# Kernel tuning notes

Measured on AMD Instinct MI355X. Metric: run time of the kernel, lower is better.

Reference implementation:

```python
import jax, jax.numpy as jnp
import numpy as np

N_USER = 50000
N_ITEM = 50000
N_EDGE = 1600000
D_IN = 64
D_OUT = 64


def _mean_agg(msgs, dst, num_dst):
    # copy_u + mean: segment-mean of edge messages onto dst nodes; zero for
    # zero-in-degree nodes (DGL default).
    s = jax.ops.segment_sum(msgs, dst, num_segments=num_dst)          # [Nd, D]
    cnt = jax.ops.segment_sum(jnp.ones((msgs.shape[0],), msgs.dtype), dst,
                              num_segments=num_dst)                    # [Nd]
    return s / jnp.maximum(cnt, 1.0)[:, None]


def setup_inputs() -> dict:
    key = jax.random.key(0)
    ks = jax.random.split(key, 12)
    return {
        'user_feat': jax.random.normal(ks[0], (N_USER, D_IN), jnp.float32),
        'item_feat': jax.random.normal(ks[1], (N_ITEM, D_IN), jnp.float32),
        'rate_src': jax.random.randint(ks[2], (N_EDGE,), 0, N_USER, jnp.int64 if jax.config.jax_enable_x64 else jnp.int32),
        'rate_dst': jax.random.randint(ks[3], (N_EDGE,), 0, N_ITEM, jnp.int64 if jax.config.jax_enable_x64 else jnp.int32),
        'rev_src': jax.random.randint(ks[4], (N_EDGE,), 0, N_ITEM, jnp.int64 if jax.config.jax_enable_x64 else jnp.int32),
        'rev_dst': jax.random.randint(ks[5], (N_EDGE,), 0, N_USER, jnp.int64 if jax.config.jax_enable_x64 else jnp.int32),
        'W_rate': jax.random.normal(ks[6], (D_IN, D_OUT), jnp.float32) * (1.0 / np.sqrt(D_IN)),
        'b_rate': jnp.zeros((D_OUT,), jnp.float32),
        'W_rev': jax.random.normal(ks[7], (D_IN, D_OUT), jnp.float32) * (1.0 / np.sqrt(D_IN)),
        'b_rev': jnp.zeros((D_OUT,), jnp.float32),
        'loop_weight': jax.random.normal(ks[8], (D_IN, D_OUT), jnp.float32) * (1.0 / np.sqrt(D_IN)),
        'h_bias': jnp.zeros((D_OUT,), jnp.float32),
    }


def reference(user_feat, item_feat, rate_src, rate_dst, rev_src, rev_dst,
              W_rate, b_rate, W_rev, b_rev, loop_weight, h_bias):
    # Per-etype Linear on source-node features (applied node-wise, as in torch).
    Wh_rate = user_feat @ W_rate + b_rate      # [Nu, Dout], etype 'rate': user->item
    Wh_rev = item_feat @ W_rev + b_rev         # [Ni, Dout], etype 'rated-by': item->user

    # copy_u + mean per etype, cross-reduce 'sum' (one etype per dst ntype here).
    h_item = _mean_agg(Wh_rate[rate_src], rate_dst, N_ITEM)
    h_user = _mean_agg(Wh_rev[rev_src], rev_dst, N_USER)

    # self-loop + bias (dropout p=0.0 is identity)
    h_user = h_user + user_feat @ loop_weight + h_bias
    h_item = h_item + item_feat @ loop_weight + h_bias
    return (h_user, h_item)
```

## Files before the change

kernel.cpp:

```cpp
#include <hip/hip_runtime.h>

#define N_USER 50000
#define N_ITEM 50000
#define N_NODE 50000
#define N_EDGE 1600000
#define D 64

#define CB_SHIFT 8
#define NBKT 196
#define BCAP 10240
#define CHUNK 8192
#define NCH ((N_EDGE + CHUNK - 1) / CHUNK)
#define NCAST 3125
#define NAGB ((N_NODE + 31) / 32)
#define SA_STR 36

typedef __attribute__((ext_vector_type(8))) short short8;
typedef __attribute__((ext_vector_type(4))) float floatx4;

__device__ __forceinline__ unsigned short f32_to_bf16(float x) {
    unsigned u = __float_as_uint(x);
    unsigned r = (u + 0x7FFFu + ((u >> 16) & 1u)) >> 16;
    return (unsigned short)r;
}
__device__ __forceinline__ unsigned pack2(float lo, float hi) {
    return (unsigned)f32_to_bf16(lo) | ((unsigned)f32_to_bf16(hi) << 16);
}

__device__ __forceinline__ void acc2(float* a, int k, unsigned u) {
    a[k]     += __uint_as_float(u << 16);
    a[k + 1] += __uint_as_float(u & 0xFFFF0000u);
}
__device__ __forceinline__ void acc8(float* a, uint4 w) {
    acc2(a, 0, w.x); acc2(a, 2, w.y); acc2(a, 4, w.z); acc2(a, 6, w.w);
}

__global__ __launch_bounds__(256) void cast_bin(
    const float4* __restrict__ fU, ushort4* __restrict__ bU,
    const float4* __restrict__ fI, ushort4* __restrict__ bI,
    const int* __restrict__ srcA, const int* __restrict__ dstA, unsigned* __restrict__ gbinA,
    const int* __restrict__ srcB, const int* __restrict__ dstB, unsigned* __restrict__ gbinB,
    int* __restrict__ fcur,
    const float* __restrict__ W_rev, const float* __restrict__ W_rate,
    const float* __restrict__ loop_w,
    unsigned short* __restrict__ wtRev, unsigned short* __restrict__ wtRate,
    unsigned short* __restrict__ wtLoop)
{
    __shared__ unsigned lbin[CHUNK];
    __shared__ int hist[NBKT];
    __shared__ int lofs[NBKT];
    __shared__ int lcur[NBKT];
    __shared__ int gbase[NBKT];
    __shared__ int sc[256];

    const int id = blockIdx.x;

    if (id >= 2 * NCH + 2 * NCAST) {
        const int which = id - (2 * NCH + 2 * NCAST);
        const float* __restrict__ Wsrc = which == 0 ? W_rev : (which == 1 ? W_rate : loop_w);
        unsigned short* __restrict__ Wdst = which == 0 ? wtRev : (which == 1 ? wtRate : wtLoop);
        for (int i = threadIdx.x; i < 4096; i += 256)
            Wdst[i] = f32_to_bf16(Wsrc[(i & 63) * 64 + (i >> 6)]);
        return;
    }

    if (id >= 2 * NCH) {
        const int cid = id - 2 * NCH;
        const int et = (cid >= NCAST) ? 1 : 0;
        const float4* __restrict__ in = et ? fI : fU;
        ushort4* __restrict__ out     = et ? bI : bU;
        int i = (cid - et * NCAST) * 256 + threadIdx.x;
        float4 v = in[i];
        ushort4 o;
        o.x = f32_to_bf16(v.x); o.y = f32_to_bf16(v.y);
        o.z = f32_to_bf16(v.z); o.w = f32_to_bf16(v.w);
        out[i] = o;
        return;
    }

    const int et = (id >= NCH) ? 1 : 0;
    const int chunk = id - et * NCH;
    const int* __restrict__ src = et ? srcB : srcA;
    const int* __restrict__ dst = et ? dstB : dstA;
    unsigned* __restrict__ gbin = et ? gbinB : gbinA;
    int* __restrict__ fc = fcur + et * NBKT;

    const int base = chunk * CHUNK;
    const int nE = min(CHUNK, N_EDGE - base);
    const int n4 = nE >> 2;
    const int4* dst4 = (const int4*)(dst + base);
    const int4* src4 = (const int4*)(src + base);
    const int tid = threadIdx.x;

    for (int i = tid; i < NBKT; i += 256) hist[i] = 0;
    __syncthreads();

    for (int i = tid; i < n4; i += 256) {
        int4 d = dst4[i];
        atomicAdd(&hist[d.x >> CB_SHIFT], 1);
        atomicAdd(&hist[d.y >> CB_SHIFT], 1);
        atomicAdd(&hist[d.z >> CB_SHIFT], 1);
        atomicAdd(&hist[d.w >> CB_SHIFT], 1);
    }
    __syncthreads();

    int v = (tid < NBKT) ? hist[tid] : 0;
    sc[tid] = v;
    __syncthreads();
    for (int o = 1; o < 256; o <<= 1) {
        int t = (tid >= o) ? sc[tid - o] : 0;
        __syncthreads();
        sc[tid] += t;
        __syncthreads();
    }
    if (tid < NBKT) {
        int excl = sc[tid] - v;
        lofs[tid] = excl;
        lcur[tid] = excl;
        gbase[tid] = v ? (tid * BCAP + atomicAdd(&fc[tid], v)) : 0;
    }
    __syncthreads();

    for (int i = tid; i < n4; i += 256) {
        int4 d = dst4[i];
        int4 s = src4[i];
        { int p = atomicAdd(&lcur[d.x >> CB_SHIFT], 1); lbin[p] = ((unsigned)d.x << 16) | (unsigned)s.x; }
        { int p = atomicAdd(&lcur[d.y >> CB_SHIFT], 1); lbin[p] = ((unsigned)d.y << 16) | (unsigned)s.y; }
        { int p = atomicAdd(&lcur[d.z >> CB_SHIFT], 1); lbin[p] = ((unsigned)d.z << 16) | (unsigned)s.z; }
        { int p = atomicAdd(&lcur[d.w >> CB_SHIFT], 1); lbin[p] = ((unsigned)d.w << 16) | (unsigned)s.w; }
    }
    __syncthreads();

    const int wv = tid >> 6, ln = tid & 63;
    for (int b = wv; b < NBKT; b += 4) {
        const int s0 = lofs[b], c = hist[b], g = gbase[b];
        for (int t = ln; t < c; t += 64) gbin[g + t] = lbin[s0 + t];
    }
}

__global__ __launch_bounds__(256) void bucket_sort(
    const unsigned* __restrict__ gbinI, unsigned short* __restrict__ srtI,
    int* __restrict__ offI, int* __restrict__ cntI,
    const unsigned* __restrict__ gbinU, unsigned short* __restrict__ srtU,
    int* __restrict__ offU, int* __restrict__ cntU,
    const int* __restrict__ fcur)
{
    const int et = blockIdx.y;
    const unsigned* __restrict__ gbin = et ? gbinU : gbinI;
    unsigned short* __restrict__ srt  = et ? srtU : srtI;
    int* __restrict__ off   = et ? offU : offI;
    int* __restrict__ cntG  = et ? cntU : cntI;
    const int b = blockIdx.x;
    const int startg = b * BCAP;
    const int n = fcur[et * NBKT + b];
    const int nodebase = b << CB_SHIFT;
    const int tid = threadIdx.x;

    __shared__ int cnt[256];
    __shared__ int sc[256];
    __shared__ int pos[256];
    __shared__ unsigned short lsrt[BCAP];

    cnt[tid] = 0;
    __syncthreads();

    for (int i = tid; i < n; i += 256)
        atomicAdd(&cnt[(int)(gbin[startg + i] >> 16) - nodebase], 1);
    __syncthreads();

    int v = cnt[tid];
    sc[tid] = v;
    __syncthreads();
    for (int o = 1; o < 256; o <<= 1) {
        int t = (tid >= o) ? sc[tid - o] : 0;
        __syncthreads();
        sc[tid] += t;
        __syncthreads();
    }
    {
        int excl = sc[tid] - v;
        pos[tid] = excl;
        int node = nodebase + tid;
        if (node < N_NODE) { off[node] = startg + excl; cntG[node] = v; }
    }
    __syncthreads();

    for (int i = tid; i < n; i += 256) {
        unsigned p = gbin[startg + i];
        int q = atomicAdd(&pos[(int)(p >> 16) - nodebase], 1);
        lsrt[q] = (unsigned short)(p & 0xFFFFu);
    }
    __syncthreads();

    for (int i = tid; i < n; i += 256) srt[startg + i] = lsrt[i];
}

__global__ __launch_bounds__(256) void agg_gemm(
    const uint4* __restrict__ userB, const uint4* __restrict__ itemB,
    const int* __restrict__ offU, const int* __restrict__ cntU, const unsigned short* __restrict__ srtU,
    const int* __restrict__ offI, const int* __restrict__ cntI, const unsigned short* __restrict__ srtI,
    const unsigned short* __restrict__ wtRev, const float* __restrict__ b_rev,
    const unsigned short* __restrict__ wtRate, const float* __restrict__ b_rate,
    const unsigned short* __restrict__ wtLoop, const float* __restrict__ h_bias,
    float* __restrict__ out)
{
    const int et = blockIdx.y;
    const uint4* __restrict__ tab = et ? userB : itemB;
    const int* __restrict__ off   = et ? offI : offU;
    const int* __restrict__ cntG  = et ? cntI : cntU;
    const unsigned short* __restrict__ srt = et ? srtI : srtU;
    const unsigned short* __restrict__ Wt  = et ? wtRate : wtRev;
    const float* __restrict__ b_et = et ? b_rate : b_rev;
    const unsigned short* __restrict__ feat =
        (const unsigned short*)(et ? itemB : userB);
    float* __restrict__ outN = out + (et ? (size_t)N_USER * D : 0);

    __shared__ unsigned sA[32][SA_STR];
    __shared__ int sCnt[32];

    const int tid = threadIdx.x;

    const int grp  = tid >> 3;
    const int lane = tid & 7;
    const int node = blockIdx.x * 32 + grp;
    const bool valid = (node < N_NODE);
    const int nd = valid ? node : (N_NODE - 1);
    const int start = off[nd];
    const int c = valid ? cntG[nd] : 0;
    const int end = start + c;

    float aA[8] = {0.f, 0.f, 0.f, 0.f, 0.f, 0.f, 0.f, 0.f};
    float aB[8] = {0.f, 0.f, 0.f, 0.f, 0.f, 0.f, 0.f, 0.f};

    int e = start;
    for (; e + 8 <= end; e += 8) {
        int s0 = (int)srt[e],     s1 = (int)srt[e + 1];
        int s2 = (int)srt[e + 2], s3 = (int)srt[e + 3];
        int s4 = (int)srt[e + 4], s5 = (int)srt[e + 5];
        int s6 = (int)srt[e + 6], s7 = (int)srt[e + 7];
        uint4 w0 = tab[(size_t)s0 * 8 + lane];
        uint4 w1 = tab[(size_t)s1 * 8 + lane];
        uint4 w2 = tab[(size_t)s2 * 8 + lane];
        uint4 w3 = tab[(size_t)s3 * 8 + lane];
        uint4 w4 = tab[(size_t)s4 * 8 + lane];
        uint4 w5 = tab[(size_t)s5 * 8 + lane];
        uint4 w6 = tab[(size_t)s6 * 8 + lane];
        uint4 w7 = tab[(size_t)s7 * 8 + lane];
        acc8(aA, w0); acc8(aB, w1); acc8(aA, w2); acc8(aB, w3);
        acc8(aA, w4); acc8(aB, w5); acc8(aA, w6); acc8(aB, w7);
    }
    for (; e + 4 <= end; e += 4) {
        int s0 = (int)srt[e],     s1 = (int)srt[e + 1];
        int s2 = (int)srt[e + 2], s3 = (int)srt[e + 3];
        uint4 w0 = tab[(size_t)s0 * 8 + lane];
        uint4 w1 = tab[(size_t)s1 * 8 + lane];
        uint4 w2 = tab[(size_t)s2 * 8 + lane];
        uint4 w3 = tab[(size_t)s3 * 8 + lane];
        acc8(aA, w0); acc8(aB, w1); acc8(aA, w2); acc8(aB, w3);
    }
    for (; e < end; ++e) {
        uint4 w = tab[(size_t)(int)srt[e] * 8 + lane];
        acc8(aA, w);
    }
    #pragma unroll
    for (int k = 0; k < 8; ++k) aA[k] += aB[k];

    const float inv = (c > 0) ? 1.0f / (float)c : 0.0f;
    sA[grp][lane * 4 + 0] = pack2(aA[0] * inv, aA[1] * inv);
    sA[grp][lane * 4 + 1] = pack2(aA[2] * inv, aA[3] * inv);
    sA[grp][lane * 4 + 2] = pack2(aA[4] * inv, aA[5] * inv);
    sA[grp][lane * 4 + 3] = pack2(aA[6] * inv, aA[7] * inv);
    if (lane == 0) sCnt[grp] = c;
    __syncthreads();

    const int wave = tid >> 6;
    const int l    = tid & 63;
    const int quad = l >> 4;
    const int l16  = l & 15;
    const int rowbase = (wave & 1) * 16;
    const int colbase = (wave >> 1) * 32;

    const int lrow = rowbase + l16;
    short8 aAgg0 = *(const short8*)&sA[lrow][     quad * 4];
    short8 aAgg1 = *(const short8*)&sA[lrow][16 + quad * 4];
    const int grow = blockIdx.x * 32 + lrow;
    const int gr = (grow < N_NODE) ? grow : (N_NODE - 1);
    short8 aFeat0 = *(const short8*)(feat + (size_t)gr * 64 +      quad * 8);
    short8 aFeat1 = *(const short8*)(feat + (size_t)gr * 64 + 32 + quad * 8);

    #pragma unroll
    for (int t = 0; t < 2; ++t) {
        const int n = colbase + t * 16 + l16;
        short8 bW0 = *(const short8*)(Wt     + n * 64 +      quad * 8);
        short8 bW1 = *(const short8*)(Wt     + n * 64 + 32 + quad * 8);
        short8 bL0 = *(const short8*)(wtLoop + n * 64 +      quad * 8);
        short8 bL1 = *(const short8*)(wtLoop + n * 64 + 32 + quad * 8);
        floatx4 a = {0.f, 0.f, 0.f, 0.f};
        a = __builtin_amdgcn_mfma_f32_16x16x32_bf16(aAgg0,  bW0, a, 0, 0, 0);
        a = __builtin_amdgcn_mfma_f32_16x16x32_bf16(aAgg1,  bW1, a, 0, 0, 0);
        a = __builtin_amdgcn_mfma_f32_16x16x32_bf16(aFeat0, bL0, a, 0, 0, 0);
        a = __builtin_amdgcn_mfma_f32_16x16x32_bf16(aFeat1, bL1, a, 0, 0, 0);
        const float bh = h_bias[n], be = b_et[n];
        #pragma unroll
        for (int i = 0; i < 4; ++i) {
            const int rl = rowbase + quad * 4 + i;
            const int r = blockIdx.x * 32 + rl;
            if (r < N_NODE) {
                outN[(size_t)r * D + n] = a[i] + bh + (sCnt[rl] > 0 ? be : 0.f);
            }
        }
    }
}

extern "C" void kernel_launch(void* const* d_in, const int* in_sizes, int n_in,
                              void* d_out, int out_size, void* d_ws, size_t ws_size,
                              hipStream_t stream)
{
    const float* user_feat = (const float*)d_in[0];
    const float* item_feat = (const float*)d_in[1];
    const int*   rate_src  = (const int*)d_in[2];
    const int*   rate_dst  = (const int*)d_in[3];
    const int*   rev_src   = (const int*)d_in[4];
    const int*   rev_dst   = (const int*)d_in[5];
    const float* W_rate    = (const float*)d_in[6];
    const float* b_rate    = (const float*)d_in[7];
    const float* W_rev     = (const float*)d_in[8];
    const float* b_rev     = (const float*)d_in[9];
    const float* loop_w    = (const float*)d_in[10];
    const float* h_bias    = (const float*)d_in[11];
    float* out = (float*)d_out;

    char* p = (char*)d_ws;
    ushort4* userB = (ushort4*)p; p += (size_t)N_USER * D * 2;
    ushort4* itemB = (ushort4*)p; p += (size_t)N_ITEM * D * 2;
    unsigned* gbinI = (unsigned*)p; p += (size_t)NBKT * BCAP * 4;
    unsigned* gbinU = (unsigned*)p; p += (size_t)NBKT * BCAP * 4;
    unsigned short* srtI = (unsigned short*)p; p += (size_t)NBKT * BCAP * 2;
    unsigned short* srtU = (unsigned short*)p; p += (size_t)NBKT * BCAP * 2;
    int* offI = (int*)p; p += (size_t)N_NODE * 4;
    int* offU = (int*)p; p += (size_t)N_NODE * 4;
    int* cntI = (int*)p; p += (size_t)N_NODE * 4;
    int* cntU = (int*)p; p += (size_t)N_NODE * 4;
    int* fcur = (int*)p; p += (size_t)(2 * NBKT) * 4;
    unsigned short* wtRev  = (unsigned short*)p; p += 4096 * 2;
    unsigned short* wtRate = (unsigned short*)p; p += 4096 * 2;
    unsigned short* wtLoop = (unsigned short*)p; p += 4096 * 2;
    (void)ws_size;

    hipMemsetAsync(fcur, 0, (size_t)(2 * NBKT) * sizeof(int), stream);

    cast_bin<<<dim3(2 * NCH + 2 * NCAST + 3), 256, 0, stream>>>(
        (const float4*)user_feat, userB, (const float4*)item_feat, itemB,
        rate_src, rate_dst, gbinI,
        rev_src,  rev_dst,  gbinU, fcur,
        W_rev, W_rate, loop_w, wtRev, wtRate, wtLoop);

    bucket_sort<<<dim3(NBKT, 2), 256, 0, stream>>>(
        gbinI, srtI, offI, cntI,
        gbinU, srtU, offU, cntU, fcur);

    agg_gemm<<<dim3(NAGB, 2), 256, 0, stream>>>(
        (const uint4*)userB, (const uint4*)itemB,
        offU, cntU, srtU,
        offI, cntI, srtI,
        wtRev, b_rev, wtRate, b_rate,
        wtLoop, h_bias, out);

    (void)in_sizes; (void)n_in; (void)out_size;
}
```

Baseline: 199.9 us.

## Fuse bucket sort into aggregation+GEMM kernel, keeping sorted edges in LDS

Merges the per-bucket counting sort and the gather/mean/MFMA GEMM kernel into one 512-thread kernel. Each bucket is handled by two blocks, each sorting the full bucket into shared memory and then aggregating its half of the nodes from LDS. This removes one kernel launch and the global round trip for the sorted source indices, offsets and counts. The cost is that every bucket is sorted twice, and the larger LDS footprint and fewer blocks lower occupancy.

```diff
diff --git a/kernel.cpp b/kernel.cpp
--- a/kernel.cpp
+++ b/kernel.cpp
@@ -12,7 +12,6 @@
 #define CHUNK 8192
 #define NCH ((N_EDGE + CHUNK - 1) / CHUNK)
 #define NCAST 3125
-#define NAGB ((N_NODE + 31) / 32)
 #define SA_STR 36
 
 typedef __attribute__((ext_vector_type(8))) short short8;
@@ -138,177 +137,153 @@
     }
 }
 
-__global__ __launch_bounds__(256) void bucket_sort(
-    const unsigned* __restrict__ gbinI, unsigned short* __restrict__ srtI,
-    int* __restrict__ offI, int* __restrict__ cntI,
-    const unsigned* __restrict__ gbinU, unsigned short* __restrict__ srtU,
-    int* __restrict__ offU, int* __restrict__ cntU,
-    const int* __restrict__ fcur)
-{
-    const int et = blockIdx.y;
-    const unsigned* __restrict__ gbin = et ? gbinU : gbinI;
-    unsigned short* __restrict__ srt  = et ? srtU : srtI;
-    int* __restrict__ off   = et ? offU : offI;
-    int* __restrict__ cntG  = et ? cntU : cntI;
-    const int b = blockIdx.x;
-    const int startg = b * BCAP;
-    const int n = fcur[et * NBKT + b];
-    const int nodebase = b << CB_SHIFT;
-    const int tid = threadIdx.x;
-
-    __shared__ int cnt[256];
-    __shared__ int sc[256];
-    __shared__ int pos[256];
-    __shared__ unsigned short lsrt[BCAP];
-
-    cnt[tid] = 0;
-    __syncthreads();
-
-    for (int i = tid; i < n; i += 256)
-        atomicAdd(&cnt[(int)(gbin[startg + i] >> 16) - nodebase], 1);
-    __syncthreads();
-
-    int v = cnt[tid];
-    sc[tid] = v;
-    __syncthreads();
-    for (int o = 1; o < 256; o <<= 1) {
-        int t = (tid >= o) ? sc[tid - o] : 0;
-        __syncthreads();
-        sc[tid] += t;
-        __syncthreads();
-    }
-    {
-        int excl = sc[tid] - v;
-        pos[tid] = excl;
-        int node = nodebase + tid;
-        if (node < N_NODE) { off[node] = startg + excl; cntG[node] = v; }
-    }
-    __syncthreads();
-
-    for (int i = tid; i < n; i += 256) {
-        unsigned p = gbin[startg + i];
-        int q = atomicAdd(&pos[(int)(p >> 16) - nodebase], 1);
-        lsrt[q] = (unsigned short)(p & 0xFFFFu);
-    }
-    __syncthreads();
-
-    for (int i = tid; i < n; i += 256) srt[startg + i] = lsrt[i];
-}
-
-__global__ __launch_bounds__(256) void agg_gemm(
+__global__ __launch_bounds__(512) void sort_agg_gemm(
     const uint4* __restrict__ userB, const uint4* __restrict__ itemB,
-    const int* __restrict__ offU, const int* __restrict__ cntU, const unsigned short* __restrict__ srtU,
-    const int* __restrict__ offI, const int* __restrict__ cntI, const unsigned short* __restrict__ srtI,
+    const unsigned* __restrict__ gbinI, const unsigned* __restrict__ gbinU,
+    const int* __restrict__ fcur,
     const unsigned short* __restrict__ wtRev, const float* __restrict__ b_rev,
     const unsigned short* __restrict__ wtRate, const float* __restrict__ b_rate,
     const unsigned short* __restrict__ wtLoop, const float* __restrict__ h_bias,
     float* __restrict__ out)
 {
     const int et = blockIdx.y;
-    const uint4* __restrict__ tab = et ? userB : itemB;
-    const int* __restrict__ off   = et ? offI : offU;
-    const int* __restrict__ cntG  = et ? cntI : cntU;
-    const unsigned short* __restrict__ srt = et ? srtI : srtU;
-    const unsigned short* __restrict__ Wt  = et ? wtRate : wtRev;
-    const float* __restrict__ b_et = et ? b_rate : b_rev;
+    const unsigned* __restrict__ gbin = et ? gbinI : gbinU;
+    const uint4* __restrict__ tab     = et ? userB : itemB;
+    const unsigned short* __restrict__ Wt = et ? wtRate : wtRev;
+    const float* __restrict__ b_et    = et ? b_rate : b_rev;
     const unsigned short* __restrict__ feat =
         (const unsigned short*)(et ? itemB : userB);
     float* __restrict__ outN = out + (et ? (size_t)N_USER * D : 0);
 
-    __shared__ unsigned sA[32][SA_STR];
-    __shared__ int sCnt[32];
-
+    const int b     = blockIdx.x >> 1;
+    const int split = blockIdx.x & 1;
+    const int n = fcur[(et ? 0 : NBKT) + b];
+    const int startg = b * BCAP;
+    const int nodebase = b << CB_SHIFT;
     const int tid = threadIdx.x;
 
-    const int grp  = tid >> 3;
-    const int lane = tid & 7;
-    const int node = blockIdx.x * 32 + grp;
-    const bool valid = (node < N_NODE);
-    const int nd = valid ? node : (N_NODE - 1);
-    const int start = off[nd];
-    const int c = valid ? cntG[nd] : 0;
-    const int end = start + c;
-
-    float aA[8] = {0.f, 0.f, 0.f, 0.f, 0.f, 0.f, 0.f, 0.f};
-    float aB[8] = {0.f, 0.f, 0.f, 0.f, 0.f, 0.f, 0.f, 0.f};
-
-    int e = start;
-    for (; e + 8 <= end; e += 8) {
-        int s0 = (int)srt[e],     s1 = (int)srt[e + 1];
-        int s2 = (int)srt[e + 2], s3 = (int)srt[e + 3];
-        int s4 = (int)srt[e + 4], s5 = (int)srt[e + 5];
-        int s6 = (int)srt[e + 6], s7 = (int)srt[e + 7];
-        uint4 w0 = tab[(size_t)s0 * 8 + lane];
-        uint4 w1 = tab[(size_t)s1 * 8 + lane];
-        uint4 w2 = tab[(size_t)s2 * 8 + lane];
-        uint4 w3 = tab[(size_t)s3 * 8 + lane];
-        uint4 w4 = tab[(size_t)s4 * 8 + lane];
-        uint4 w5 = tab[(size_t)s5 * 8 + lane];
-        uint4 w6 = tab[(size_t)s6 * 8 + lane];
-        uint4 w7 = tab[(size_t)s7 * 8 + lane];
-        acc8(aA, w0); acc8(aB, w1); acc8(aA, w2); acc8(aB, w3);
-        acc8(aA, w4); acc8(aB, w5); acc8(aA, w6); acc8(aB, w7);
-    }
-    for (; e + 4 <= end; e += 4) {
-        int s0 = (int)srt[e],     s1 = (int)srt[e + 1];
-        int s2 = (int)srt[e + 2], s3 = (int)srt[e + 3];
-        uint4 w0 = tab[(size_t)s0 * 8 + lane];
-        uint4 w1 = tab[(size_t)s1 * 8 + lane];
-        uint4 w2 = tab[(size_t)s2 * 8 + lane];
-        uint4 w3 = tab[(size_t)s3 * 8 + lane];
-        acc8(aA, w0); acc8(aB, w1); acc8(aA, w2); acc8(aB, w3);
-    }
-    for (; e < end; ++e) {
-        uint4 w = tab[(size_t)(int)srt[e] * 8 + lane];
-        acc8(aA, w);
-    }
-    #pragma unroll
-    for (int k = 0; k < 8; ++k) aA[k] += aB[k];
-
-    const float inv = (c > 0) ? 1.0f / (float)c : 0.0f;
-    sA[grp][lane * 4 + 0] = pack2(aA[0] * inv, aA[1] * inv);
-    sA[grp][lane * 4 + 1] = pack2(aA[2] * inv, aA[3] * inv);
-    sA[grp][lane * 4 + 2] = pack2(aA[4] * inv, aA[5] * inv);
-    sA[grp][lane * 4 + 3] = pack2(aA[6] * inv, aA[7] * inv);
-    if (lane == 0) sCnt[grp] = c;
-    __syncthreads();
-
-    const int wave = tid >> 6;
-    const int l    = tid & 63;
-    const int quad = l >> 4;
-    const int l16  = l & 15;
-    const int rowbase = (wave & 1) * 16;
-    const int colbase = (wave >> 1) * 32;
-
-    const int lrow = rowbase + l16;
-    short8 aAgg0 = *(const short8*)&sA[lrow][     quad * 4];
-    short8 aAgg1 = *(const short8*)&sA[lrow][16 + quad * 4];
-    const int grow = blockIdx.x * 32 + lrow;
-    const int gr = (grow < N_NODE) ? grow : (N_NODE - 1);
-    short8 aFeat0 = *(const short8*)(feat + (size_t)gr * 64 +      quad * 8);
-    short8 aFeat1 = *(const short8*)(feat + (size_t)gr * 64 + 32 + quad * 8);
-
-    #pragma unroll
-    for (int t = 0; t < 2; ++t) {
-        const int n = colbase + t * 16 + l16;
-        short8 bW0 = *(const short8*)(Wt     + n * 64 +      quad * 8);
-        short8 bW1 = *(const short8*)(Wt     + n * 64 + 32 + quad * 8);
-        short8 bL0 = *(const short8*)(wtLoop + n * 64 +      quad * 8);
-        short8 bL1 = *(const short8*)(wtLoop + n * 64 + 32 + quad * 8);
-        floatx4 a = {0.f, 0.f, 0.f, 0.f};
-        a = __builtin_amdgcn_mfma_f32_16x16x32_bf16(aAgg0,  bW0, a, 0, 0, 0);
-        a = __builtin_amdgcn_mfma_f32_16x16x32_bf16(aAgg1,  bW1, a, 0, 0, 0);
-        a = __builtin_amdgcn_mfma_f32_16x16x32_bf16(aFeat0, bL0, a, 0, 0, 0);
-        a = __builtin_amdgcn_mfma_f32_16x16x32_bf16(aFeat1, bL1, a, 0, 0, 0);
-        const float bh = h_bias[n], be = b_et[n];
+    __shared__ unsigned short lsrt[BCAP];
+    __shared__ int scnt[256];
+    __shared__ int soff[256];
+    __shared__ int pos[256];
+    __shared__ int sc[256];
+    __shared__ unsigned sA[64][SA_STR];
+
+    if (tid < 256) scnt[tid] = 0;
+    __syncthreads();
+
+    for (int i = tid; i < n; i += 512)
+        atomicAdd(&scnt[(int)(gbin[startg + i] >> 16) - nodebase], 1);
+    __syncthreads();
+
+    int v = 0;
+    if (tid < 256) { v = scnt[tid]; sc[tid] = v; }
+    __syncthreads();
+    for (int o = 1; o < 256; o <<= 1) {
+        int t = 0;
+        if (tid < 256 && tid >= o) t = sc[tid - o];
+        __syncthreads();
+        if (tid < 256) sc[tid] += t;
+        __syncthreads();
+    }
+    if (tid < 256) { soff[tid] = sc[tid] - v; pos[tid] = sc[tid] - v; }
+    __syncthreads();
+
+    for (int i = tid; i < n; i += 512) {
+        unsigned p = gbin[startg + i];
+        int q = atomicAdd(&pos[(int)(p >> 16) - nodebase], 1);
+        lsrt[q] = (unsigned short)(p & 0xFFFFu);
+    }
+    __syncthreads();
+
+    const int grp = tid >> 3;
+    const int dl  = tid & 7;
+    const int wave = tid >> 6, l = tid & 63, quad = l >> 4, l16 = l & 15;
+    const int rowbase = (wave & 3) * 16;
+    const int colbase = (wave >> 2) * 32;
+
+    for (int r = 0; r < 2; ++r) {
+        const int lnode = split * 128 + r * 64 + grp;
+        const int start = soff[lnode];
+        const int c     = scnt[lnode];
+        const int end   = start + c;
+
+        float aA[8] = {0.f, 0.f, 0.f, 0.f, 0.f, 0.f, 0.f, 0.f};
+        float aB[8] = {0.f, 0.f, 0.f, 0.f, 0.f, 0.f, 0.f, 0.f};
+
+        int e = start;
+        for (; e + 8 <= end; e += 8) {
+            int s0 = (int)lsrt[e],     s1 = (int)lsrt[e + 1];
+            int s2 = (int)lsrt[e + 2], s3 = (int)lsrt[e + 3];
+            int s4 = (int)lsrt[e + 4], s5 = (int)lsrt[e + 5];
+            int s6 = (int)lsrt[e + 6], s7 = (int)lsrt[e + 7];
+            uint4 w0 = tab[(size_t)s0 * 8 + dl];
+            uint4 w1 = tab[(size_t)s1 * 8 + dl];
+            uint4 w2 = tab[(size_t)s2 * 8 + dl];
+            uint4 w3 = tab[(size_t)s3 * 8 + dl];
+            uint4 w4 = tab[(size_t)s4 * 8 + dl];
+            uint4 w5 = tab[(size_t)s5 * 8 + dl];
+            uint4 w6 = tab[(size_t)s6 * 8 + dl];
+            uint4 w7 = tab[(size_t)s7 * 8 + dl];
+            acc8(aA, w0); acc8(aB, w1); acc8(aA, w2); acc8(aB, w3);
+            acc8(aA, w4); acc8(aB, w5); acc8(aA, w6); acc8(aB, w7);
+        }
+        for (; e + 4 <= end; e += 4) {
+            int s0 = (int)lsrt[e],     s1 = (int)lsrt[e + 1];
+            int s2 = (int)lsrt[e + 2], s3 = (int)lsrt[e + 3];
+            uint4 w0 = tab[(size_t)s0 * 8 + dl];
+            uint4 w1 = tab[(size_t)s1 * 8 + dl];
+            uint4 w2 = tab[(size_t)s2 * 8 + dl];
+            uint4 w3 = tab[(size_t)s3 * 8 + dl];
+            acc8(aA, w0); acc8(aB, w1); acc8(aA, w2); acc8(aB, w3);
+        }
+        for (; e < end; ++e) {
+            uint4 w = tab[(size_t)(int)lsrt[e] * 8 + dl];
+            acc8(aA, w);
+        }
         #pragma unroll
-        for (int i = 0; i < 4; ++i) {
-            const int rl = rowbase + quad * 4 + i;
-            const int r = blockIdx.x * 32 + rl;
-            if (r < N_NODE) {
-                outN[(size_t)r * D + n] = a[i] + bh + (sCnt[rl] > 0 ? be : 0.f);
+        for (int k = 0; k < 8; ++k) aA[k] += aB[k];
+
+        const float inv = (c > 0) ? 1.0f / (float)c : 0.0f;
+        sA[grp][dl * 4 + 0] = pack2(aA[0] * inv, aA[1] * inv);
+        sA[grp][dl * 4 + 1] = pack2(aA[2] * inv, aA[3] * inv);
+        sA[grp][dl * 4 + 2] = pack2(aA[4] * inv, aA[5] * inv);
+        sA[grp][dl * 4 + 3] = pack2(aA[6] * inv, aA[7] * inv);
+        __syncthreads();
+
+        const int lrow = rowbase + l16;
+        short8 aAgg0 = *(const short8*)&sA[lrow][     quad * 4];
+        short8 aAgg1 = *(const short8*)&sA[lrow][16 + quad * 4];
+        const int growb = nodebase + split * 128 + r * 64;
+        const int grow = growb + lrow;
+        const int gr = (grow < N_NODE) ? grow : (N_NODE - 1);
+        short8 aFeat0 = *(const short8*)(feat + (size_t)gr * 64 +      quad * 8);
+        short8 aFeat1 = *(const short8*)(feat + (size_t)gr * 64 + 32 + quad * 8);
+
+        #pragma unroll
+        for (int t = 0; t < 2; ++t) {
+            const int nn = colbase + t * 16 + l16;
+            short8 bW0 = *(const short8*)(Wt     + nn * 64 +      quad * 8);
+            short8 bW1 = *(const short8*)(Wt     + nn * 64 + 32 + quad * 8);
+            short8 bL0 = *(const short8*)(wtLoop + nn * 64 +      quad * 8);
+            short8 bL1 = *(const short8*)(wtLoop + nn * 64 + 32 + quad * 8);
+            floatx4 a = {0.f, 0.f, 0.f, 0.f};
+            a = __builtin_amdgcn_mfma_f32_16x16x32_bf16(aAgg0,  bW0, a, 0, 0, 0);
+            a = __builtin_amdgcn_mfma_f32_16x16x32_bf16(aAgg1,  bW1, a, 0, 0, 0);
+            a = __builtin_amdgcn_mfma_f32_16x16x32_bf16(aFeat0, bL0, a, 0, 0, 0);
+            a = __builtin_amdgcn_mfma_f32_16x16x32_bf16(aFeat1, bL1, a, 0, 0, 0);
+            const float bh = h_bias[nn], be = b_et[nn];
+            #pragma unroll
+            for (int i = 0; i < 4; ++i) {
+                const int rl = rowbase + quad * 4 + i;
+                const int rglob = growb + rl;
+                if (rglob < N_NODE) {
+                    const int rc = scnt[split * 128 + r * 64 + rl];
+                    outN[(size_t)rglob * D + nn] = a[i] + bh + (rc > 0 ? be : 0.f);
+                }
             }
         }
+        __syncthreads();
     }
 }
 
@@ -335,12 +310,6 @@
     ushort4* itemB = (ushort4*)p; p += (size_t)N_ITEM * D * 2;
     unsigned* gbinI = (unsigned*)p; p += (size_t)NBKT * BCAP * 4;
     unsigned* gbinU = (unsigned*)p; p += (size_t)NBKT * BCAP * 4;
-    unsigned short* srtI = (unsigned short*)p; p += (size_t)NBKT * BCAP * 2;
-    unsigned short* srtU = (unsigned short*)p; p += (size_t)NBKT * BCAP * 2;
-    int* offI = (int*)p; p += (size_t)N_NODE * 4;
-    int* offU = (int*)p; p += (size_t)N_NODE * 4;
-    int* cntI = (int*)p; p += (size_t)N_NODE * 4;
-    int* cntU = (int*)p; p += (size_t)N_NODE * 4;
     int* fcur = (int*)p; p += (size_t)(2 * NBKT) * 4;
     unsigned short* wtRev  = (unsigned short*)p; p += 4096 * 2;
     unsigned short* wtRate = (unsigned short*)p; p += 4096 * 2;
@@ -355,14 +324,9 @@
         rev_src,  rev_dst,  gbinU, fcur,
         W_rev, W_rate, loop_w, wtRev, wtRate, wtLoop);
 
-    bucket_sort<<<dim3(NBKT, 2), 256, 0, stream>>>(
-        gbinI, srtI, offI, cntI,
-        gbinU, srtU, offU, cntU, fcur);
-
-    agg_gemm<<<dim3(NAGB, 2), 256, 0, stream>>>(
+    sort_agg_gemm<<<dim3(NBKT * 2, 2), 512, 0, stream>>>(
         (const uint4*)userB, (const uint4*)itemB,
-        offU, cntU, srtU,
-        offI, cntI, srtI,
+        gbinI, gbinU, fcur,
         wtRev, b_rev, wtRate, b_rate,
         wtLoop, h_bias, out);
 
```

After: 207.5 us. 1.04x slower.
